# Kernel tuning notes

Hardware: AMD Instinct MI355X
Metric: run time of the kernel (lower is better)

## Reference

```python
import jax, jax.numpy as jnp
import numpy as np
from jax import lax

KERNEL_SIZE = 11
DATA_RANGE = 1603.64208984375 - 1396.9390869140625


def build_gauss_kernel(size=11, sigma=1.0, n_channels=1):
    # Faithful replication of the torch helper (including its quirks):
    # gaussian(x) = exp((x-c)^2 / (-2 sigma^2)) ** 2, and the kernel is the
    # SUM of the two coordinate gaussians (np.sum over axis=2), normalized.
    grid = np.float32(np.mgrid[0:size, 0:size].T)  # (size, size, 2)

    def gaussian(x):
        return np.exp((x - size // 2) ** 2 / (-2 * sigma ** 2)) ** 2

    kernel = np.sum(gaussian(grid), axis=2)
    kernel /= np.sum(kernel)
    kernel = np.tile(kernel, (n_channels, 1, 1))  # (C, size, size)
    return jnp.asarray(kernel[:, None, :, :], dtype=jnp.float32)  # (C,1,k,k)


def _dwconv(x, w, pad):
    # depthwise conv, NCHW / OIHW, groups = channels (here 1)
    return lax.conv_general_dilated(
        x, w, window_strides=(1, 1), padding=[(pad, pad), (pad, pad)],
        dimension_numbers=("NCHW", "OIHW", "NCHW"),
        feature_group_count=x.shape[1])


def setup_inputs() -> dict:
    key = jax.random.key(0)
    k1, k2 = jax.random.split(key)
    B, C, H, W = 32, 1, 512, 512
    preds = jax.random.normal(k1, (B, C, H, W), dtype=jnp.float32)
    target = jax.random.normal(k2, (B, C, H, W), dtype=jnp.float32)
    window = build_gauss_kernel(KERNEL_SIZE, sigma=1.0, n_channels=C)
    return {"preds": preds, "target": target, "window": window}


def reference(preds, target, window):
    img1 = preds.astype(jnp.float32)
    img2 = target.astype(jnp.float32)
    C1 = (0.01 * DATA_RANGE) ** 2
    C2 = (0.03 * DATA_RANGE) ** 2
    pad = KERNEL_SIZE // 2

    mu1 = _dwconv(img1, window, pad)
    mu2 = _dwconv(img2, window, pad)
    mu1_sq = mu1 * mu1
    mu2_sq = mu2 * mu2
    mu1_mu2 = mu1 * mu2
    sigma1_sq = _dwconv(img1 * img1, window, pad) - mu1_sq
    sigma2_sq = _dwconv(img2 * img2, window, pad) - mu2_sq
    sigma12 = _dwconv(img1 * img2, window, pad) - mu1_mu2

    ssim_map = ((2 * mu1_mu2 + C1) * (2 * sigma12 + C2)) / (
        (mu1_sq + mu2_sq + C1) * (sigma1_sq + sigma2_sq + C2))
    return ssim_map.mean()  # average=True
```

## Files before the change

kernel.cpp:

```cpp
#include <hip/hip_runtime.h>


#define TH 16
#define TW 64
#define ICOLS 74
#define IS 76
#define VUNITS (ICOLS * 4)
#define NBLOCKS 8192

__device__ __forceinline__ float rfl_f32(float x) {
    return __uint_as_float(
        (unsigned)__builtin_amdgcn_readfirstlane((int)__float_as_uint(x)));
}

__device__ __forceinline__ unsigned pack_bf16(float a, float b) {
    unsigned ua = (__float_as_uint(a) + 0x8000u) & 0xffff0000u;
    unsigned ub = (__float_as_uint(b) + 0x8000u) >> 16;
    return ua | ub;
}

__global__ __launch_bounds__(256, 4) void ssim_kernel(
    const float* __restrict__ x1, const float* __restrict__ x2,
    const float* __restrict__ win, float* __restrict__ part)
{
    __shared__ __align__(16) unsigned sp[5][TH][IS];
    __shared__ float partials[4];

    const int tid = threadIdx.x;
    const int tile_c0 = blockIdx.x * TW;
    const int tile_r0 = blockIdx.y * TH;
    const float* __restrict__ img1 = x1 + (size_t)blockIdx.z * (512 * 512);
    const float* __restrict__ img2 = x2 + (size_t)blockIdx.z * (512 * 512);

    float u[11];
    {
        float u0 = rfl_f32(win[0]) * 0.5f;
#pragma unroll
        for (int i = 0; i < 11; ++i)
            u[i] = (i == 0) ? u0 : (rfl_f32(win[i * 11]) - u0);
    }

    auto mathstore = [&](int rr0, int c, const float* V1, const float* V2) {
        float bx[5];
        float dd[3][5];
        float gg[4][5];
#pragma unroll
        for (int ch = 0; ch < 5; ++ch) {
            bx[ch] = 0.f;
#pragma unroll
            for (int j = 0; j < 3; ++j) dd[j][ch] = 0.f;
#pragma unroll
            for (int r = 0; r < 4; ++r) gg[r][ch] = 0.f;
        }
#pragma unroll
        for (int k = 0; k < 14; ++k) {
            float v1 = V1[k], v2 = V2[k];
            float p[5];
            p[0] = v1; p[1] = v2;
            p[2] = v1 * v1; p[3] = v2 * v2; p[4] = v1 * v2;
            if (k < 11) {
#pragma unroll
                for (int ch = 0; ch < 5; ++ch) bx[ch] += p[ch];
            }
            if (k < 3) {
#pragma unroll
                for (int ch = 0; ch < 5; ++ch) dd[k][ch] = -p[ch];
            }
            if (k >= 11) {
#pragma unroll
                for (int ch = 0; ch < 5; ++ch) dd[k - 11][ch] += p[ch];
            }
#pragma unroll
            for (int r = 0; r < 4; ++r) {
                if (k >= r + 4 && k <= r + 6) {
                    float w = u[k - r];
#pragma unroll
                    for (int ch = 0; ch < 5; ++ch)
                        gg[r][ch] = fmaf(w, p[ch], gg[r][ch]);
                }
            }
        }
#pragma unroll
        for (int r = 0; r < 4; ++r) {
#pragma unroll
            for (int ch = 0; ch < 5; ++ch)
                sp[ch][rr0 + r][c] = pack_bf16(gg[r][ch], bx[ch]);
            if (r < 3) {
#pragma unroll
                for (int ch = 0; ch < 5; ++ch) bx[ch] += dd[r][ch];
            }
        }
    };

    const bool interior = (blockIdx.y >= 1) && (blockIdx.y <= 30) &&
                          (blockIdx.x >= 1) && (blockIdx.x <= 6);

    if (interior) {
        for (int unit = tid; unit < VUNITS; unit += 256) {
            int seg = unit / ICOLS, c = unit - seg * ICOLS, rr0 = seg * 4;
            const float* q1 = img1 + (tile_r0 + rr0 - 5) * 512 + (tile_c0 + c - 5);
            const float* q2 = img2 + (tile_r0 + rr0 - 5) * 512 + (tile_c0 + c - 5);
            float V1[14], V2[14];
#pragma unroll
            for (int k = 0; k < 14; ++k) { V1[k] = q1[k * 512]; V2[k] = q2[k * 512]; }
            mathstore(rr0, c, V1, V2);
        }
    } else {
        for (int unit = tid; unit < VUNITS; unit += 256) {
            int seg = unit / ICOLS, c = unit - seg * ICOLS, rr0 = seg * 4;
            int gc = tile_c0 + c - 5;
            int gcc = min(max(gc, 0), 511);
            float mc = ((unsigned)gc < 512u) ? 1.0f : 0.0f;
            int gr0 = tile_r0 + rr0 - 5;
            float V1[14], V2[14];
#pragma unroll
            for (int k = 0; k < 14; ++k) {
                int gr = gr0 + k;
                int grc = min(max(gr, 0), 511);
                float m = ((unsigned)gr < 512u) ? mc : 0.0f;
                int off = grc * 512 + gcc;
                V1[k] = img1[off] * m;
                V2[k] = img2[off] * m;
            }
            mathstore(rr0, c, V1, V2);
        }
    }
    __syncthreads();

    float local = 0.0f;
    {
        int r = tid >> 4;
        int cg = (tid & 15) * 4;

        float conv[5][4];
#pragma unroll
        for (int ch = 0; ch < 5; ++ch) {
            const uint4* p = (const uint4*)&sp[ch][r][cg];
            uint4 w0 = p[0], w1 = p[1], w2 = p[2];
            unsigned wc = ((const unsigned*)&sp[ch][r][cg])[12];
            unsigned wd = ((const unsigned*)&sp[ch][r][cg])[13];

            float gv[14], bv[10];
            gv[0]  = __uint_as_float(w0.x & 0xffff0000u);
            gv[1]  = __uint_as_float(w0.y & 0xffff0000u);
            gv[2]  = __uint_as_float(w0.z & 0xffff0000u);
            gv[3]  = __uint_as_float(w0.w & 0xffff0000u);
            gv[4]  = __uint_as_float(w1.x & 0xffff0000u);
            gv[5]  = __uint_as_float(w1.y & 0xffff0000u);
            gv[6]  = __uint_as_float(w1.z & 0xffff0000u);
            gv[7]  = __uint_as_float(w1.w & 0xffff0000u);
            gv[8]  = __uint_as_float(w2.x & 0xffff0000u);
            gv[9]  = __uint_as_float(w2.y & 0xffff0000u);
            gv[10] = __uint_as_float(w2.z & 0xffff0000u);
            gv[11] = __uint_as_float(w2.w & 0xffff0000u);
            gv[12] = __uint_as_float(wc & 0xffff0000u);
            gv[13] = __uint_as_float(wd & 0xffff0000u);
            bv[4]  = __uint_as_float(w1.x << 16);
            bv[5]  = __uint_as_float(w1.y << 16);
            bv[6]  = __uint_as_float(w1.z << 16);
            bv[7]  = __uint_as_float(w1.w << 16);
            bv[8]  = __uint_as_float(w2.x << 16);
            bv[9]  = __uint_as_float(w2.y << 16);

            float hs = 0.f;
#pragma unroll
            for (int j = 0; j < 11; ++j) hs += gv[j];
#pragma unroll
            for (int k = 0; k < 4; ++k) {
                float gs = u[4] * bv[k + 4];
                gs = fmaf(u[5], bv[k + 5], gs);
                gs = fmaf(u[6], bv[k + 6], gs);
                conv[ch][k] = hs + gs;
                if (k < 3) hs += gv[k + 11] - gv[k];
            }
        }

        constexpr double DR = 1603.64208984375 - 1396.9390869140625;
        constexpr float C1 = (float)((0.01 * DR) * (0.01 * DR));
        constexpr float C2 = (float)((0.03 * DR) * (0.03 * DR));
#pragma unroll
        for (int k = 0; k < 4; ++k) {
            float mu1 = conv[0][k], mu2 = conv[1][k];
            float e11 = conv[2][k], e22 = conv[3][k], e12 = conv[4][k];
            float mu1s = mu1 * mu1, mu2s = mu2 * mu2, mu12 = mu1 * mu2;
            float s1 = e11 - mu1s, s2 = e22 - mu2s, s12 = e12 - mu12;
            float num = (2.f * mu12 + C1) * (2.f * s12 + C2);
            float den = (mu1s + mu2s + C1) * (s1 + s2 + C2);
            local = fmaf(num, __builtin_amdgcn_rcpf(den), local);
        }
    }

#pragma unroll
    for (int off = 32; off > 0; off >>= 1) local += __shfl_down(local, off);
    if ((tid & 63) == 0) partials[tid >> 6] = local;
    __syncthreads();
    if (tid == 0) {
        int bidx = blockIdx.x + 8 * (blockIdx.y + 32 * blockIdx.z);
        part[bidx] = partials[0] + partials[1] + partials[2] + partials[3];
    }
}

__global__ __launch_bounds__(256) void reduce_kernel(
    const float* __restrict__ part, float* __restrict__ out)
{
    __shared__ float partials[4];
    float s = 0.0f;
    int tid = threadIdx.x;
#pragma unroll
    for (int i = 0; i < NBLOCKS / 256; ++i)
        s += part[tid + i * 256];
#pragma unroll
    for (int off = 32; off > 0; off >>= 1) s += __shfl_down(s, off);
    if ((tid & 63) == 0) partials[tid >> 6] = s;
    __syncthreads();
    if (tid == 0) {
        float t = partials[0] + partials[1] + partials[2] + partials[3];
        out[0] = t * (1.0f / 8388608.0f);
    }
}

extern "C" void kernel_launch(void* const* d_in, const int* in_sizes, int n_in,
                              void* d_out, int out_size, void* d_ws, size_t ws_size,
                              hipStream_t stream) {
    const float* preds  = (const float*)d_in[0];
    const float* target = (const float*)d_in[1];
    const float* window = (const float*)d_in[2];
    float* out = (float*)d_out;
    float* part = (float*)d_ws;

    dim3 grid(512 / TW, 512 / TH, 32);
    ssim_kernel<<<grid, 256, 0, stream>>>(preds, target, window, part);
    reduce_kernel<<<1, 256, 0, stream>>>(part, out);
}
```

Before: 118.2 us.

## Use hardware bf16 pack, skip mask on unpack, raise occupancy, vectorize reduce

Replaces the manual bf16 rounding pack with the v_cvt_pk_bf16_f32 instruction and drops the masking of the high half when unpacking, which leaves the low bf16 bits as extra mantissa noise in the g values. Raises the launch-bounds occupancy hint from 4 to 6 blocks per CU. Adds a fast path in border tiles for columns and rows that lie fully inside the image, so they skip clamping and masking. Vectorizes the final reduction with float4 loads. These trim ALU work in the packing, unpacking and border paths, but the higher occupancy hint may force register spills.

Result: no change. 116.7 us (-1.3%).

```diff
diff --git a/kernel.cpp b/kernel.cpp
--- a/kernel.cpp
+++ b/kernel.cpp
@@ -13,13 +13,13 @@
         (unsigned)__builtin_amdgcn_readfirstlane((int)__float_as_uint(x)));
 }
 
-__device__ __forceinline__ unsigned pack_bf16(float a, float b) {
-    unsigned ua = (__float_as_uint(a) + 0x8000u) & 0xffff0000u;
-    unsigned ub = (__float_as_uint(b) + 0x8000u) >> 16;
-    return ua | ub;
-}
-
-__global__ __launch_bounds__(256, 4) void ssim_kernel(
+__device__ __forceinline__ unsigned pack_pair(float g, float b) {
+    unsigned r;
+    asm("v_cvt_pk_bf16_f32 %0, %1, %2" : "=v"(r) : "v"(b), "v"(g));
+    return r;
+}
+
+__global__ __launch_bounds__(256, 6) void ssim_kernel(
     const float* __restrict__ x1, const float* __restrict__ x2,
     const float* __restrict__ win, float* __restrict__ part)
 {
@@ -84,7 +84,7 @@
         for (int r = 0; r < 4; ++r) {
 #pragma unroll
             for (int ch = 0; ch < 5; ++ch)
-                sp[ch][rr0 + r][c] = pack_bf16(gg[r][ch], bx[ch]);
+                sp[ch][rr0 + r][c] = pack_pair(gg[r][ch], bx[ch]);
             if (r < 3) {
 #pragma unroll
                 for (int ch = 0; ch < 5; ++ch) bx[ch] += dd[r][ch];
@@ -109,18 +109,25 @@
         for (int unit = tid; unit < VUNITS; unit += 256) {
             int seg = unit / ICOLS, c = unit - seg * ICOLS, rr0 = seg * 4;
             int gc = tile_c0 + c - 5;
-            int gcc = min(max(gc, 0), 511);
-            float mc = ((unsigned)gc < 512u) ? 1.0f : 0.0f;
             int gr0 = tile_r0 + rr0 - 5;
             float V1[14], V2[14];
-#pragma unroll
-            for (int k = 0; k < 14; ++k) {
-                int gr = gr0 + k;
-                int grc = min(max(gr, 0), 511);
-                float m = ((unsigned)gr < 512u) ? mc : 0.0f;
-                int off = grc * 512 + gcc;
-                V1[k] = img1[off] * m;
-                V2[k] = img2[off] * m;
+            if (((unsigned)gc < 512u) && ((unsigned)gr0 <= 498u)) {
+                const float* q1 = img1 + gr0 * 512 + gc;
+                const float* q2 = img2 + gr0 * 512 + gc;
+#pragma unroll
+                for (int k = 0; k < 14; ++k) { V1[k] = q1[k * 512]; V2[k] = q2[k * 512]; }
+            } else {
+                int gcc = min(max(gc, 0), 511);
+                float mc = ((unsigned)gc < 512u) ? 1.0f : 0.0f;
+#pragma unroll
+                for (int k = 0; k < 14; ++k) {
+                    int gr = gr0 + k;
+                    int grc = min(max(gr, 0), 511);
+                    float m = ((unsigned)gr < 512u) ? mc : 0.0f;
+                    int off = grc * 512 + gcc;
+                    V1[k] = img1[off] * m;
+                    V2[k] = img2[off] * m;
+                }
             }
             mathstore(rr0, c, V1, V2);
         }
@@ -141,20 +148,20 @@
             unsigned wd = ((const unsigned*)&sp[ch][r][cg])[13];
 
             float gv[14], bv[10];
-            gv[0]  = __uint_as_float(w0.x & 0xffff0000u);
-            gv[1]  = __uint_as_float(w0.y & 0xffff0000u);
-            gv[2]  = __uint_as_float(w0.z & 0xffff0000u);
-            gv[3]  = __uint_as_float(w0.w & 0xffff0000u);
-            gv[4]  = __uint_as_float(w1.x & 0xffff0000u);
-            gv[5]  = __uint_as_float(w1.y & 0xffff0000u);
-            gv[6]  = __uint_as_float(w1.z & 0xffff0000u);
-            gv[7]  = __uint_as_float(w1.w & 0xffff0000u);
-            gv[8]  = __uint_as_float(w2.x & 0xffff0000u);
-            gv[9]  = __uint_as_float(w2.y & 0xffff0000u);
-            gv[10] = __uint_as_float(w2.z & 0xffff0000u);
-            gv[11] = __uint_as_float(w2.w & 0xffff0000u);
-            gv[12] = __uint_as_float(wc & 0xffff0000u);
-            gv[13] = __uint_as_float(wd & 0xffff0000u);
+            gv[0]  = __uint_as_float(w0.x);
+            gv[1]  = __uint_as_float(w0.y);
+            gv[2]  = __uint_as_float(w0.z);
+            gv[3]  = __uint_as_float(w0.w);
+            gv[4]  = __uint_as_float(w1.x);
+            gv[5]  = __uint_as_float(w1.y);
+            gv[6]  = __uint_as_float(w1.z);
+            gv[7]  = __uint_as_float(w1.w);
+            gv[8]  = __uint_as_float(w2.x);
+            gv[9]  = __uint_as_float(w2.y);
+            gv[10] = __uint_as_float(w2.z);
+            gv[11] = __uint_as_float(w2.w);
+            gv[12] = __uint_as_float(wc);
+            gv[13] = __uint_as_float(wd);
             bv[4]  = __uint_as_float(w1.x << 16);
             bv[5]  = __uint_as_float(w1.y << 16);
             bv[6]  = __uint_as_float(w1.z << 16);
@@ -206,9 +213,12 @@
     __shared__ float partials[4];
     float s = 0.0f;
     int tid = threadIdx.x;
-#pragma unroll
-    for (int i = 0; i < NBLOCKS / 256; ++i)
-        s += part[tid + i * 256];
+    const float4* p4 = (const float4*)part;
+#pragma unroll
+    for (int i = 0; i < NBLOCKS / 1024; ++i) {
+        float4 v = p4[tid + i * 256];
+        s += (v.x + v.y) + (v.z + v.w);
+    }
 #pragma unroll
     for (int off = 32; off > 0; off >>= 1) s += __shfl_down(s, off);
     if ((tid & 63) == 0) partials[tid >> 6] = s;
```
